# Kernel tuning notes

Hardware: AMD Instinct MI355X
Metric: run time of the kernel (lower is better)

The kernel has to match this reference:

```python
import jax, jax.numpy as jnp
import numpy as np

N, IN_F, H, D = 4096, 256, 4, 64  # nodes, in_features, num_heads, head_dim
NEG_BIG = -9e15


def setup_inputs() -> dict:
    key = jax.random.key(0)
    k1, k2, k3, k4, k5 = jax.random.split(key, 5)
    x = jax.random.normal(k1, (N, IN_F), dtype=jnp.float32)
    adj = jax.random.randint(k2, (N, N), 0, 2, dtype=jnp.int32)
    # xavier-uniform-scale init for W: [in_features, H*D]
    lim_w = float(np.sqrt(6.0 / (IN_F + H * D)))
    W = jax.random.uniform(k3, (IN_F, H * D), minval=-lim_w, maxval=lim_w, dtype=jnp.float32)
    # a: [2*D, 1] split into a1 (dest half) and a2 (source half)
    lim_a = float(np.sqrt(6.0 / (2 * D + 1)))
    a1 = jax.random.uniform(k4, (D,), minval=-lim_a, maxval=lim_a, dtype=jnp.float32)
    a2 = jax.random.uniform(k5, (D,), minval=-lim_a, maxval=lim_a, dtype=jnp.float32)
    return {"x": x, "adj": adj, "W": W, "a1": a1, "a2": a2}


def reference(x, adj, W, a1, a2):
    n = x.shape[0]
    h = (x @ W).reshape(n, H, D)                      # [N, H, D]
    # e[i,j,h] = leaky_relu(<h_i, a1> + <h_j, a2>)  (== concat([h_i,h_j]) @ a)
    si = jnp.einsum("nhd,d->nh", h, a1)               # [N, H]
    sj = jnp.einsum("nhd,d->nh", h, a2)               # [N, H]
    e = jax.nn.leaky_relu(si[:, None, :] + sj[None, :, :], negative_slope=0.2)
    e = jnp.where(adj[:, :, None] > 0, e, NEG_BIG)    # mask non-edges
    att = jax.nn.softmax(e, axis=1)                   # softmax over neighbors j
    out = jnp.einsum("ijh,jhd->ihd", att, h)          # per-head aggregation
    return out.reshape(n, H * D)                      # concat heads
```

## Files before the change

### kernel.cpp

```cpp
#include <hip/hip_runtime.h>
#include <hip/hip_bf16.h>


typedef __bf16 bf16x8 __attribute__((ext_vector_type(8)));
typedef float floatx4 __attribute__((ext_vector_type(4)));

#define LOG2E 1.4426950408889634f
#define NN 4096

__device__ __forceinline__ void gl16(const void* g, void* l) {
  __builtin_amdgcn_global_load_lds(
      (const __attribute__((address_space(1))) unsigned int*)g,
      (__attribute__((address_space(3))) unsigned int*)l, 16, 0, 0);
}

__global__ __launch_bounds__(256) void gat_pack(const int* __restrict__ adj,
                                                unsigned char* __restrict__ adjb) {
  int T = blockIdx.x * 256 + threadIdx.x;
  const int stride = 2048 * 256;
#pragma unroll
  for (int it = 0; it < 4; ++it, T += stride) {
    const int* p = adj + (size_t)T * 8;
    int4 a = *(const int4*)p;
    int4 b = *(const int4*)(p + 4);
    unsigned int m = 0;
    m |= (a.x != 0) ? 1u : 0u;
    m |= (a.y != 0) ? 2u : 0u;
    m |= (a.z != 0) ? 4u : 0u;
    m |= (a.w != 0) ? 8u : 0u;
    m |= (b.x != 0) ? 16u : 0u;
    m |= (b.y != 0) ? 32u : 0u;
    m |= (b.z != 0) ? 64u : 0u;
    m |= (b.w != 0) ? 128u : 0u;
    adjb[T] = (unsigned char)m;
  }
}

__global__ __launch_bounds__(256) void gat_prep(
    const float* __restrict__ x, const float* __restrict__ W,
    const float* __restrict__ a1, const float* __restrict__ a2,
    __bf16* __restrict__ hT, float* __restrict__ siT, float2* __restrict__ vv2T,
    float* __restrict__ sjm) {
  __shared__ float hl[32 * 68];
  __shared__ float sjb[32];
  const int t = threadIdx.x;
  const int it = blockIdx.x, hh = blockIdx.y;
  const int i0 = it * 32, c0 = hh * 64;
  const int tr = t >> 4, tc = t & 15;

  float acc[2][4] = {{0.f,0.f,0.f,0.f},{0.f,0.f,0.f,0.f}};
  const float* xr = x + (size_t)(i0 + tr * 2) * 256;
  const float* wp = W + c0 + tc * 4;
  for (int k = 0; k < 256; k += 4) {
    float4 xv0 = *(const float4*)(xr + k);
    float4 xv1 = *(const float4*)(xr + 256 + k);
    float xs[2][4] = {{xv0.x, xv0.y, xv0.z, xv0.w},
                      {xv1.x, xv1.y, xv1.z, xv1.w}};
#pragma unroll
    for (int kk = 0; kk < 4; ++kk) {
      float4 wv = *(const float4*)(wp + (size_t)(k + kk) * 256);
#pragma unroll
      for (int i = 0; i < 2; ++i) {
        acc[i][0] = fmaf(xs[i][kk], wv.x, acc[i][0]);
        acc[i][1] = fmaf(xs[i][kk], wv.y, acc[i][1]);
        acc[i][2] = fmaf(xs[i][kk], wv.z, acc[i][2]);
        acc[i][3] = fmaf(xs[i][kk], wv.w, acc[i][3]);
      }
    }
  }

  float4 a1v = *(const float4*)(a1 + tc * 4);
  float4 a2v = *(const float4*)(a2 + tc * 4);
#pragma unroll
  for (int i = 0; i < 2; ++i) {
    float s1 = acc[i][0]*a1v.x + acc[i][1]*a1v.y + acc[i][2]*a1v.z + acc[i][3]*a1v.w;
    float s2 = acc[i][0]*a2v.x + acc[i][1]*a2v.y + acc[i][2]*a2v.z + acc[i][3]*a2v.w;
#pragma unroll
    for (int off = 1; off < 16; off <<= 1) {
      s1 += __shfl_xor(s1, off);
      s2 += __shfl_xor(s2, off);
    }
    if (tc == 0) {
      int r = tr * 2 + i;
      siT[hh * NN + i0 + r] = s1 * LOG2E;
      float sjs = s2 * LOG2E;
      vv2T[hh * NN + i0 + r] =
          make_float2(__builtin_amdgcn_exp2f(sjs), __builtin_amdgcn_exp2f(0.2f * sjs));
      sjb[r] = sjs;
    }
    *(float4*)&hl[(tr * 2 + i) * 68 + tc * 4] =
        make_float4(acc[i][0], acc[i][1], acc[i][2], acc[i][3]);
  }
  __syncthreads();

  if (t < 32) {
    float v = sjb[t];
#pragma unroll
    for (int off = 1; off < 32; off <<= 1) v = fmaxf(v, __shfl_xor(v, off));
    if (t == 0) sjm[it * 4 + hh] = v;
  }

  const int d = t & 63, g = t >> 6;
  bf16x8 h0;
#pragma unroll
  for (int ii = 0; ii < 8; ++ii) h0[ii] = (__bf16)hl[(g * 8 + ii) * 68 + d];
  *(bf16x8*)(hT + (size_t)(hh * 64 + d) * NN + i0 + g * 8) = h0;
}

__global__ __launch_bounds__(256, 2) void gat_attn(
    const __bf16* __restrict__ hT, const float* __restrict__ siT,
    const float2* __restrict__ vv2T, const float* __restrict__ sjm,
    const unsigned int* __restrict__ adjw,
    float* __restrict__ pacc, float* __restrict__ pl) {
  __shared__ __align__(16) char lds[35328];
  const int t = threadIdx.x;
  const int w = t >> 6, lane = t & 63, quad = lane >> 4, l16 = lane & 15;
  const int i0 = blockIdx.x * 64, hh = blockIdx.y, s = blockIdx.z;
  const int jbeg = s * 2048;

  const __bf16* hTw = hT + (size_t)hh * 64 * NN + jbeg + w * 32 + quad * 8;
  const float2* vw = vv2T + hh * NN + jbeg;

  int hoff[4];
#pragma unroll
  for (int nt = 0; nt < 4; ++nt) hoff[nt] = (nt * 16 + l16) * NN;

  const unsigned int* mp[4];
#pragma unroll
  for (int mt = 0; mt < 4; ++mt)
    mp[mt] = adjw + (size_t)(i0 + mt * 16 + l16) * 128 + (jbeg >> 5) + w;

#pragma unroll
  for (int nt = 0; nt < 4; ++nt)
    gl16(hTw + hoff[nt], lds + ((w * 4 + nt) << 10) + (lane << 4));
  if (w == 0) gl16(vw + lane * 2, lds + 32768 + (lane << 4));
  unsigned int mc[4], mn[4];
#pragma unroll
  for (int mt = 0; mt < 4; ++mt) mc[mt] = mp[mt][0];

  float vv = fmaxf(sjm[lane * 4 + hh], sjm[(lane + 64) * 4 + hh]);
#pragma unroll
  for (int off = 1; off < 64; off <<= 1) vv = fmaxf(vv, __shfl_xor(vv, off));
  float u[4], u2[4];
#pragma unroll
  for (int mt = 0; mt < 4; ++mt) {
    float sis = siT[hh * NN + i0 + mt * 16 + l16];
    float tt = sis + vv;
    float m = fmaxf(tt, 0.2f * tt);
    u[mt] = __builtin_amdgcn_exp2f(sis - m);
    u2[mt] = __builtin_amdgcn_exp2f(0.2f * sis - m);
  }

  bf16x8 ones;
#pragma unroll
  for (int ii = 0; ii < 8; ++ii) ones[ii] = (__bf16)1.0f;

  floatx4 zv = {0.f, 0.f, 0.f, 0.f};
  floatx4 acc[4][4], lacc[4];
#pragma unroll
  for (int mt = 0; mt < 4; ++mt) {
    lacc[mt] = zv;
#pragma unroll
    for (int nt = 0; nt < 4; ++nt) acc[mt][nt] = zv;
  }

  __syncthreads();

  for (int win = 0; win < 16; ++win) {
    const int p = win & 1;
    const char* hb = lds + (p << 14);
    const char* vb = lds + 32768 + (p << 10);

    if (win + 1 < 16) {
#pragma unroll
      for (int mt = 0; mt < 4; ++mt) mn[mt] = mp[mt][(win + 1) * 4];
      const int jn = (win + 1) << 7;
      char* hbn = lds + ((p ^ 1) << 14);
#pragma unroll
      for (int nt = 0; nt < 4; ++nt)
        gl16(hTw + hoff[nt] + jn, hbn + ((w * 4 + nt) << 10) + (lane << 4));
      if (w == 0)
        gl16(vw + jn + lane * 2, lds + 32768 + ((p ^ 1) << 10) + (lane << 4));
    }

    bf16x8 bfr[4];
#pragma unroll
    for (int nt = 0; nt < 4; ++nt)
      bfr[nt] = *(const bf16x8*)(hb + ((w * 4 + nt) << 10) + (lane << 4));
    float4 q[4];
#pragma unroll
    for (int c = 0; c < 4; ++c)
      q[c] = *(const float4*)(vb + (w << 8) + (quad << 6) + (c << 4));

#pragma unroll
    for (int mt = 0; mt < 4; ++mt) {
      unsigned int m8 = mc[mt] >> (quad * 8);
      bf16x8 af;
#pragma unroll
      for (int c = 0; c < 4; ++c) {
        float p0 = fmaxf(u[mt] * q[c].x, u2[mt] * q[c].y);
        float p1 = fmaxf(u[mt] * q[c].z, u2[mt] * q[c].w);
        int b0 = ((int)(m8 << (31 - 2 * c))) >> 31;
        int b1 = ((int)(m8 << (30 - 2 * c))) >> 31;
        af[2 * c]     = (__bf16)__uint_as_float(__float_as_uint(p0) & (unsigned)b0);
        af[2 * c + 1] = (__bf16)__uint_as_float(__float_as_uint(p1) & (unsigned)b1);
      }
#pragma unroll
      for (int nt = 0; nt < 4; ++nt)
        acc[mt][nt] = __builtin_amdgcn_mfma_f32_16x16x32_bf16(af, bfr[nt],
                                                              acc[mt][nt], 0, 0, 0);
      lacc[mt] = __builtin_amdgcn_mfma_f32_16x16x32_bf16(af, ones, lacc[mt], 0, 0, 0);
    }
#pragma unroll
    for (int mt = 0; mt < 4; ++mt) mc[mt] = mn[mt];
    __syncthreads();
  }

  float* accs = (float*)lds;
  float* lsum = (float*)(lds + 34816);
  if (w < 2) {
#pragma unroll
    for (int mt = 0; mt < 4; ++mt)
#pragma unroll
      for (int reg = 0; reg < 4; ++reg) {
        int row = mt * 16 + quad * 4 + reg;
        float* ap = accs + (w * 64 + row) * 68;
#pragma unroll
        for (int nt = 0; nt < 4; ++nt)
          ap[nt * 16 + l16] = acc[mt][nt][reg];
        if (l16 == 0) lsum[w * 64 + row] = lacc[mt][reg];
      }
  }
  __syncthreads();
  if (w >= 2) {
    const int b = w - 2;
#pragma unroll
    for (int mt = 0; mt < 4; ++mt)
#pragma unroll
      for (int reg = 0; reg < 4; ++reg) {
        int row = mt * 16 + quad * 4 + reg;
        float* ap = accs + (b * 64 + row) * 68;
#pragma unroll
        for (int nt = 0; nt < 4; ++nt)
          ap[nt * 16 + l16] += acc[mt][nt][reg];
        if (l16 == 0) lsum[b * 64 + row] += lacc[mt][reg];
      }
  }
  __syncthreads();

  const int r = t >> 2, cb = (t & 3) * 16;
  float* op = pacc + (size_t)s * NN * 256 + (size_t)(i0 + r) * 256 + hh * 64 + cb;
#pragma unroll
  for (int c4 = 0; c4 < 4; ++c4) {
    int c = cb + c4 * 4;
    float4 o;
    o.x = accs[r * 68 + c + 0] + accs[(64 + r) * 68 + c + 0];
    o.y = accs[r * 68 + c + 1] + accs[(64 + r) * 68 + c + 1];
    o.z = accs[r * 68 + c + 2] + accs[(64 + r) * 68 + c + 2];
    o.w = accs[r * 68 + c + 3] + accs[(64 + r) * 68 + c + 3];
    *(float4*)(op + c4 * 4) = o;
  }
  if (t < 64)
    pl[(size_t)s * NN * 4 + (i0 + t) * 4 + hh] = lsum[t] + lsum[64 + t];
}

__global__ __launch_bounds__(256) void gat_reduce(
    const float* __restrict__ pacc, const float* __restrict__ pl,
    float* __restrict__ out) {
  const int e4 = blockIdx.x * 256 + threadIdx.x;
  const int e = e4 * 4;
  const int i = e >> 8;
  const int h = (e & 255) >> 6;
  float4 a0 = *(const float4*)(pacc + e);
  float4 a1 = *(const float4*)(pacc + (size_t)NN * 256 + e);
  float l = pl[i * 4 + h] + pl[(size_t)NN * 4 + i * 4 + h];
  float inv = 1.0f / l;
  *(float4*)(out + e) = make_float4((a0.x + a1.x) * inv, (a0.y + a1.y) * inv,
                                    (a0.z + a1.z) * inv, (a0.w + a1.w) * inv);
}

extern "C" void kernel_launch(void* const* d_in, const int* in_sizes, int n_in,
                              void* d_out, int out_size, void* d_ws, size_t ws_size,
                              hipStream_t stream) {
  const float* x  = (const float*)d_in[0];
  const int*   adj = (const int*)d_in[1];
  const float* W  = (const float*)d_in[2];
  const float* a1 = (const float*)d_in[3];
  const float* a2 = (const float*)d_in[4];
  float* out = (float*)d_out;
  char* ws = (char*)d_ws;

  __bf16* hT   = (__bf16*)ws;
  float*  siT  = (float*)(ws + 2097152);
  float2* vv2T = (float2*)(ws + 2162688);
  float*  sjm  = (float*)(ws + 2293760);
  unsigned char* adjb = (unsigned char*)(ws + 2295808);
  float*  pacc = (float*)(ws + 4392960);
  float*  pl   = (float*)(ws + 12781568);

  gat_pack<<<2048, 256, 0, stream>>>(adj, adjb);
  gat_prep<<<dim3(128, 4), 256, 0, stream>>>(x, W, a1, a2, hT, siT, vv2T, sjm);
  gat_attn<<<dim3(64, 4, 2), 256, 0, stream>>>(hT, siT, vv2T, sjm,
                                               (const unsigned int*)adjb, pacc, pl);
  gat_reduce<<<1024, 256, 0, stream>>>(pacc, pl, out);
}
```

Before: 165.1 us.

## Fuse adjacency packing into prep, pre-swizzle h tiles, and double window size

Merges the adjacency bit-packing kernel into the projection kernel as extra blocks, removing one launch and letting the two run concurrently. The projection now writes h in a fragment-ready tiled layout, so the attention kernel loads contiguous 4KB chunks straight into LDS instead of strided rows. The attention loop processes 256 columns per window, which halves the number of barriers, and it reads the vv2 values directly into registers rather than staging them in LDS. LDS per block grows to 64KB, which may limit occupancy.

```diff
diff --git a/kernel.cpp b/kernel.cpp
--- a/kernel.cpp
+++ b/kernel.cpp
@@ -14,37 +14,40 @@
       (__attribute__((address_space(3))) unsigned int*)l, 16, 0, 0);
 }
 
-__global__ __launch_bounds__(256) void gat_pack(const int* __restrict__ adj,
-                                                unsigned char* __restrict__ adjb) {
-  int T = blockIdx.x * 256 + threadIdx.x;
-  const int stride = 2048 * 256;
-#pragma unroll
-  for (int it = 0; it < 4; ++it, T += stride) {
-    const int* p = adj + (size_t)T * 8;
-    int4 a = *(const int4*)p;
-    int4 b = *(const int4*)(p + 4);
-    unsigned int m = 0;
-    m |= (a.x != 0) ? 1u : 0u;
-    m |= (a.y != 0) ? 2u : 0u;
-    m |= (a.z != 0) ? 4u : 0u;
-    m |= (a.w != 0) ? 8u : 0u;
-    m |= (b.x != 0) ? 16u : 0u;
-    m |= (b.y != 0) ? 32u : 0u;
-    m |= (b.z != 0) ? 64u : 0u;
-    m |= (b.w != 0) ? 128u : 0u;
-    adjb[T] = (unsigned char)m;
-  }
-}
-
 __global__ __launch_bounds__(256) void gat_prep(
     const float* __restrict__ x, const float* __restrict__ W,
     const float* __restrict__ a1, const float* __restrict__ a2,
-    __bf16* __restrict__ hT, float* __restrict__ siT, float2* __restrict__ vv2T,
-    float* __restrict__ sjm) {
+    const int* __restrict__ adj, __bf16* __restrict__ hTf,
+    float* __restrict__ siT, float2* __restrict__ vv2T, float* __restrict__ sjm,
+    unsigned char* __restrict__ adjb) {
+  const int b = blockIdx.x;
+  const int t = threadIdx.x;
+
+  if (b >= 512) {
+    int T = (b - 512) * 256 + t;
+    const int stride = 2048 * 256;
+#pragma unroll
+    for (int it = 0; it < 4; ++it, T += stride) {
+      const int* p = adj + (size_t)T * 8;
+      int4 a = *(const int4*)p;
+      int4 bb = *(const int4*)(p + 4);
+      unsigned int m = 0;
+      m |= (a.x != 0) ? 1u : 0u;
+      m |= (a.y != 0) ? 2u : 0u;
+      m |= (a.z != 0) ? 4u : 0u;
+      m |= (a.w != 0) ? 8u : 0u;
+      m |= (bb.x != 0) ? 16u : 0u;
+      m |= (bb.y != 0) ? 32u : 0u;
+      m |= (bb.z != 0) ? 64u : 0u;
+      m |= (bb.w != 0) ? 128u : 0u;
+      adjb[T] = (unsigned char)m;
+    }
+    return;
+  }
+
   __shared__ float hl[32 * 68];
   __shared__ float sjb[32];
-  const int t = threadIdx.x;
-  const int it = blockIdx.x, hh = blockIdx.y;
+  const int it = b & 127, hh = b >> 7;
   const int i0 = it * 32, c0 = hh * 64;
   const int tr = t >> 4, tc = t & 15;
 
@@ -100,43 +103,50 @@
     if (t == 0) sjm[it * 4 + hh] = v;
   }
 
-  const int d = t & 63, g = t >> 6;
+  const int nt = t >> 6, lane = t & 63, quad = lane >> 4, l16 = lane & 15;
   bf16x8 h0;
 #pragma unroll
-  for (int ii = 0; ii < 8; ++ii) h0[ii] = (__bf16)hl[(g * 8 + ii) * 68 + d];
-  *(bf16x8*)(hT + (size_t)(hh * 64 + d) * NN + i0 + g * 8) = h0;
+  for (int jj = 0; jj < 8; ++jj)
+    h0[jj] = (__bf16)hl[(quad * 8 + jj) * 68 + nt * 16 + l16];
+  *(bf16x8*)((char*)hTf + ((((size_t)hh * 128 + it) * 4 + nt) << 10) + (lane << 4)) = h0;
 }
 
 __global__ __launch_bounds__(256, 2) void gat_attn(
-    const __bf16* __restrict__ hT, const float* __restrict__ siT,
+    const __bf16* __restrict__ hTf, const float* __restrict__ siT,
     const float2* __restrict__ vv2T, const float* __restrict__ sjm,
     const unsigned int* __restrict__ adjw,
     float* __restrict__ pacc, float* __restrict__ pl) {
-  __shared__ __align__(16) char lds[35328];
+  __shared__ __align__(16) char lds[65536];
   const int t = threadIdx.x;
   const int w = t >> 6, lane = t & 63, quad = lane >> 4, l16 = lane & 15;
   const int i0 = blockIdx.x * 64, hh = blockIdx.y, s = blockIdx.z;
   const int jbeg = s * 2048;
 
-  const __bf16* hTw = hT + (size_t)hh * 64 * NN + jbeg + w * 32 + quad * 8;
-  const float2* vw = vv2T + hh * NN + jbeg;
-
-  int hoff[4];
-#pragma unroll
-  for (int nt = 0; nt < 4; ++nt) hoff[nt] = (nt * 16 + l16) * NN;
+  const char* hsrc = (const char*)hTf +
+      (((size_t)hh * 128 + (jbeg >> 5) + w * 2) << 12) + (lane << 4);
+  const float2* vw = vv2T + (size_t)hh * NN + jbeg + w * 64;
 
   const unsigned int* mp[4];
 #pragma unroll
   for (int mt = 0; mt < 4; ++mt)
-    mp[mt] = adjw + (size_t)(i0 + mt * 16 + l16) * 128 + (jbeg >> 5) + w;
-
-#pragma unroll
-  for (int nt = 0; nt < 4; ++nt)
-    gl16(hTw + hoff[nt], lds + ((w * 4 + nt) << 10) + (lane << 4));
-  if (w == 0) gl16(vw + lane * 2, lds + 32768 + (lane << 4));
-  unsigned int mc[4], mn[4];
-#pragma unroll
-  for (int mt = 0; mt < 4; ++mt) mc[mt] = mp[mt][0];
+    mp[mt] = adjw + (size_t)(i0 + mt * 16 + l16) * 128 + (jbeg >> 5) + w * 2;
+
+  uint2 mc[4], mn[4];
+  float4 qc[2][4], qn[2][4];
+#pragma unroll
+  for (int mt = 0; mt < 4; ++mt) mc[mt] = *(const uint2*)mp[mt];
+#pragma unroll
+  for (int k = 0; k < 2; ++k) {
+    const float4* qp = (const float4*)(vw + k * 32 + quad * 8);
+#pragma unroll
+    for (int c = 0; c < 4; ++c) qc[k][c] = qp[c];
+  }
+#pragma unroll
+  for (int k = 0; k < 2; ++k)
+#pragma unroll
+    for (int nt = 0; nt < 4; ++nt)
+      gl16(hsrc + ((k * 4 + nt) << 10),
+           lds + (((w * 8 + k * 4 + nt) << 10) + (lane << 4)));
 
   float vv = fmaxf(sjm[lane * 4 + hh], sjm[(lane + 64) * 4 + hh]);
 #pragma unroll
@@ -166,53 +176,62 @@
 
   __syncthreads();
 
-  for (int win = 0; win < 16; ++win) {
+  for (int win = 0; win < 8; ++win) {
     const int p = win & 1;
-    const char* hb = lds + (p << 14);
-    const char* vb = lds + 32768 + (p << 10);
-
-    if (win + 1 < 16) {
-#pragma unroll
-      for (int mt = 0; mt < 4; ++mt) mn[mt] = mp[mt][(win + 1) * 4];
-      const int jn = (win + 1) << 7;
-      char* hbn = lds + ((p ^ 1) << 14);
+    const char* hb = lds + p * 32768;
+
+    if (win + 1 < 8) {
+#pragma unroll
+      for (int mt = 0; mt < 4; ++mt)
+        mn[mt] = *(const uint2*)(mp[mt] + (win + 1) * 8);
+#pragma unroll
+      for (int k = 0; k < 2; ++k) {
+        const float4* qp = (const float4*)(vw + (win + 1) * 256 + k * 32 + quad * 8);
+#pragma unroll
+        for (int c = 0; c < 4; ++c) qn[k][c] = qp[c];
+      }
+      char* hbn = lds + (p ^ 1) * 32768;
+      const char* hs = hsrc + (win + 1) * 32768;
+#pragma unroll
+      for (int k = 0; k < 2; ++k)
+#pragma unroll
+        for (int nt = 0; nt < 4; ++nt)
+          gl16(hs + ((k * 4 + nt) << 10),
+               hbn + (((w * 8 + k * 4 + nt) << 10) + (lane << 4)));
+    }
+
+#pragma unroll
+    for (int k = 0; k < 2; ++k) {
+      bf16x8 bfr[4];
 #pragma unroll
       for (int nt = 0; nt < 4; ++nt)
-        gl16(hTw + hoff[nt] + jn, hbn + ((w * 4 + nt) << 10) + (lane << 4));
-      if (w == 0)
-        gl16(vw + jn + lane * 2, lds + 32768 + ((p ^ 1) << 10) + (lane << 4));
-    }
-
-    bf16x8 bfr[4];
-#pragma unroll
-    for (int nt = 0; nt < 4; ++nt)
-      bfr[nt] = *(const bf16x8*)(hb + ((w * 4 + nt) << 10) + (lane << 4));
-    float4 q[4];
-#pragma unroll
-    for (int c = 0; c < 4; ++c)
-      q[c] = *(const float4*)(vb + (w << 8) + (quad << 6) + (c << 4));
-
-#pragma unroll
-    for (int mt = 0; mt < 4; ++mt) {
-      unsigned int m8 = mc[mt] >> (quad * 8);
-      bf16x8 af;
-#pragma unroll
-      for (int c = 0; c < 4; ++c) {
-        float p0 = fmaxf(u[mt] * q[c].x, u2[mt] * q[c].y);
-        float p1 = fmaxf(u[mt] * q[c].z, u2[mt] * q[c].w);
-        int b0 = ((int)(m8 << (31 - 2 * c))) >> 31;
-        int b1 = ((int)(m8 << (30 - 2 * c))) >> 31;
-        af[2 * c]     = (__bf16)__uint_as_float(__float_as_uint(p0) & (unsigned)b0);
-        af[2 * c + 1] = (__bf16)__uint_as_float(__float_as_uint(p1) & (unsigned)b1);
-      }
-#pragma unroll
-      for (int nt = 0; nt < 4; ++nt)
-        acc[mt][nt] = __builtin_amdgcn_mfma_f32_16x16x32_bf16(af, bfr[nt],
-                                                              acc[mt][nt], 0, 0, 0);
-      lacc[mt] = __builtin_amdgcn_mfma_f32_16x16x32_bf16(af, ones, lacc[mt], 0, 0, 0);
+        bfr[nt] = *(const bf16x8*)(hb + ((w * 8 + k * 4 + nt) << 10) + (lane << 4));
+#pragma unroll
+      for (int mt = 0; mt < 4; ++mt) {
+        unsigned int m8 = (k ? mc[mt].y : mc[mt].x) >> (quad * 8);
+        bf16x8 af;
+#pragma unroll
+        for (int c = 0; c < 4; ++c) {
+          float p0 = fmaxf(u[mt] * qc[k][c].x, u2[mt] * qc[k][c].y);
+          float p1 = fmaxf(u[mt] * qc[k][c].z, u2[mt] * qc[k][c].w);
+          int b0 = ((int)(m8 << (31 - 2 * c))) >> 31;
+          int b1 = ((int)(m8 << (30 - 2 * c))) >> 31;
+          af[2 * c]     = (__bf16)__uint_as_float(__float_as_uint(p0) & (unsigned)b0);
+          af[2 * c + 1] = (__bf16)__uint_as_float(__float_as_uint(p1) & (unsigned)b1);
+        }
+#pragma unroll
+        for (int nt = 0; nt < 4; ++nt)
+          acc[mt][nt] = __builtin_amdgcn_mfma_f32_16x16x32_bf16(af, bfr[nt],
+                                                                acc[mt][nt], 0, 0, 0);
+        lacc[mt] = __builtin_amdgcn_mfma_f32_16x16x32_bf16(af, ones, lacc[mt], 0, 0, 0);
+      }
     }
 #pragma unroll
     for (int mt = 0; mt < 4; ++mt) mc[mt] = mn[mt];
+#pragma unroll
+    for (int k = 0; k < 2; ++k)
+#pragma unroll
+      for (int c = 0; c < 4; ++c) qc[k][c] = qn[k][c];
     __syncthreads();
   }
 
@@ -233,17 +252,17 @@
   }
   __syncthreads();
   if (w >= 2) {
-    const int b = w - 2;
+    const int bb = w - 2;
 #pragma unroll
     for (int mt = 0; mt < 4; ++mt)
 #pragma unroll
       for (int reg = 0; reg < 4; ++reg) {
         int row = mt * 16 + quad * 4 + reg;
-        float* ap = accs + (b * 64 + row) * 68;
+        float* ap = accs + (bb * 64 + row) * 68;
 #pragma unroll
         for (int nt = 0; nt < 4; ++nt)
           ap[nt * 16 + l16] += acc[mt][nt][reg];
-        if (l16 == 0) lsum[b * 64 + row] += lacc[mt][reg];
+        if (l16 == 0) lsum[bb * 64 + row] += lacc[mt][reg];
       }
   }
   __syncthreads();
@@ -290,7 +309,7 @@
   float* out = (float*)d_out;
   char* ws = (char*)d_ws;
 
-  __bf16* hT   = (__bf16*)ws;
+  __bf16* hTf  = (__bf16*)ws;
   float*  siT  = (float*)(ws + 2097152);
   float2* vv2T = (float2*)(ws + 2162688);
   float*  sjm  = (float*)(ws + 2293760);
@@ -298,9 +317,8 @@
   float*  pacc = (float*)(ws + 4392960);
   float*  pl   = (float*)(ws + 12781568);
 
-  gat_pack<<<2048, 256, 0, stream>>>(adj, adjb);
-  gat_prep<<<dim3(128, 4), 256, 0, stream>>>(x, W, a1, a2, hT, siT, vv2T, sjm);
-  gat_attn<<<dim3(64, 4, 2), 256, 0, stream>>>(hT, siT, vv2T, sjm,
+  gat_prep<<<2560, 256, 0, stream>>>(x, W, a1, a2, adj, hTf, siT, vv2T, sjm, adjb);
+  gat_attn<<<dim3(64, 4, 2), 256, 0, stream>>>(hTf, siT, vv2T, sjm,
                                                (const unsigned int*)adjb, pacc, pl);
   gat_reduce<<<1024, 256, 0, stream>>>(pacc, pl, out);
 }
```

Result: faster. 157.2 us (-4.8%).
